# Kernel optimization log

Measured on AMD Instinct MI355X. Metric: run time of the kernel, lower is better.

The kernel has to match this reference:

```python
import jax, jax.numpy as jnp
import numpy as np

B, C, F, COUP, NBL = 8192, 512, 8, 1024, 2
D1 = C - C // 2   # 256, split_len1 (FrEIA AllInOneBlock)
D2 = C // 2       # 256, split_len2
CLAMP = 2.0       # FrEIA affine clamping default
G_INIT = 0.2 * np.log(np.exp(5.0) - 1.0)  # param init s.t. global scale activation == 1.0


def setup_inputs() -> dict:
    key = jax.random.key(0)
    ks = jax.random.split(key, 10)
    z0 = jax.random.normal(ks[0], (B, C), jnp.float32)
    # random orthogonal soft-permutation matrix per flow (permute_soft=True)
    A = jax.random.normal(ks[1], (F, C, C), jnp.float32)
    Wp, _ = jnp.linalg.qr(A)
    g = jnp.float32(G_INIT) + 0.05 * jax.random.normal(ks[2], (F, C), jnp.float32)
    off = 0.01 * jax.random.normal(ks[3], (F, C), jnp.float32)
    s0 = np.float32(1.0 / np.sqrt(D1))
    sh = np.float32(1.0 / np.sqrt(COUP))
    w0 = s0 * jax.random.normal(ks[4], (F, COUP, D1), jnp.float32)
    b0 = s0 * jax.random.normal(ks[5], (F, COUP), jnp.float32)
    wh = sh * jax.random.normal(ks[6], (F, NBL, COUP, COUP), jnp.float32)
    bh = sh * jax.random.normal(ks[7], (F, NBL, COUP), jnp.float32)
    wo = sh * jax.random.normal(ks[8], (F, 2 * D2, COUP), jnp.float32)
    bo = sh * jax.random.normal(ks[9], (F, 2 * D2), jnp.float32)
    return dict(z0=z0, Wp=Wp, g=g, off=off, w0=w0, b0=b0, wh=wh, bh=bh, wo=wo, bo=bo)


def _subnet(x1, w0, b0, wh, bh, wo, bo):
    # Linear(D1, COUP) -> ReLU -> [Linear(COUP, COUP) -> ReLU]*NBL -> Linear(COUP, 2*D2)
    h = jax.nn.relu(x1 @ w0.T + b0)
    for i in range(NBL):
        h = jax.nn.relu(h @ wh[i].T + bh[i])
    return h @ wo.T + bo


def reference(z0, Wp, g, off, w0, b0, wh, bh, wo, bo):
    def block(carry, p):
        x, ld = carry
        Wp_, g_, off_, w0_, b0_, wh_, bh_, wo_, bo_ = p
        # global affine: scale = 0.1 * softplus_{beta=0.5}(g) = 0.2 * softplus(0.5*g)
        scale = 0.2 * jax.nn.softplus(0.5 * g_)
        x = (x * scale + off_) @ Wp_.T            # soft permutation: F.linear(x, W)
        x1, x2 = x[:, :D1], x[:, D1:]
        a = 0.1 * _subnet(x1, w0_, b0_, wh_, bh_, wo_, bo_)
        s = CLAMP * jnp.tanh(a[:, :D2])
        t = a[:, D2:]
        x2 = x2 * jnp.exp(s) + t
        ld = ld + jnp.sum(s, axis=1) + jnp.sum(jnp.log(scale))
        return (jnp.concatenate([x1, x2], axis=1), ld), None

    init = (z0, jnp.zeros((z0.shape[0],), z0.dtype))
    (zk, log_det), _ = jax.lax.scan(block, init, (Wp, g, off, w0, b0, wh, bh, wo, bo))
    return zk, log_det
```

## Files before the change

### kernel.cpp

```cpp
#include <hip/hip_runtime.h>
#include <stdint.h>
#include <stddef.h>

#define B_    8192
#define C_    512
#define F_    8
#define COUP_ 1024
#define NBL_  2
#define D1_   256
#define D2_   256

typedef __attribute__((ext_vector_type(8))) short   short8;
typedef __attribute__((ext_vector_type(4))) float   floatx4;
typedef __attribute__((ext_vector_type(8))) int     int8v;
typedef __attribute__((ext_vector_type(4))) int     int4v;

__device__ __forceinline__ unsigned short f2bf(float f) {
  unsigned int u = __float_as_uint(f);
  unsigned int r = (u + 0x7fffu + ((u >> 16) & 1u)) >> 16;
  return (unsigned short)r;
}

#if __has_builtin(__builtin_amdgcn_cvt_pk_fp8_f32)
__device__ __forceinline__ unsigned char f2fp8(float f) {
  return (unsigned char)(__builtin_amdgcn_cvt_pk_fp8_f32(f, f, 0, false) & 0xFF);
}
__device__ __forceinline__ unsigned int f2fp8x4(float4 v) {
  int r = __builtin_amdgcn_cvt_pk_fp8_f32(v.x, v.y, 0, false);
  r = __builtin_amdgcn_cvt_pk_fp8_f32(v.z, v.w, r, true);
  return (unsigned int)r;
}
#else
__device__ __forceinline__ unsigned char f2fp8(float f) {
  unsigned int fu = __float_as_uint(f);
  unsigned char s = (unsigned char)((fu >> 24) & 0x80u);
  float a = fabsf(f);
  if (!(a >= 0.015625f)) {
    int m = (int)rintf(a * 512.0f);
    return s | (unsigned char)m;
  }
  if (a > 448.0f) return s | 0x7E;
  unsigned int u = __float_as_uint(a);
  int e = (int)((u >> 23) & 0xFF) - 127;
  unsigned int mant = u & 0x7FFFFFu;
  unsigned int r = mant >> 20;
  unsigned int rest = mant & 0xFFFFFu;
  if (rest > 0x80000u || (rest == 0x80000u && (r & 1u))) r++;
  if (r == 8u) { r = 0u; e++; }
  if (e > 8) { e = 8; r = 7u; }
  return s | (unsigned char)(((unsigned)(e + 7) << 3) | r);
}
__device__ __forceinline__ unsigned int f2fp8x4(float4 v) {
  uchar4 o;
  o.x = f2fp8(v.x); o.y = f2fp8(v.y); o.z = f2fp8(v.z); o.w = f2fp8(v.w);
  return *(unsigned int*)&o;
}
#endif

__device__ __forceinline__ void gload_lds16(const void* g, void* l) {
  void* gnc = const_cast<void*>(g);
  __builtin_amdgcn_global_load_lds(
      (__attribute__((address_space(1))) void*)gnc,
      (__attribute__((address_space(3))) void*)l, 16, 0, 0);
}

__device__ __forceinline__ int8v read_frag8(const unsigned char* lbase, int rr, int q) {
  const int j  = rr & 7;
  const int c0 = (2 * q) ^ j;
  const unsigned char* b = lbase + (rr >> 3) * 1024 + j * 128;
  int4v lo = *(const int4v*)(b + c0 * 16);
  int4v hi = *(const int4v*)(b + (c0 ^ 1) * 16);
  return __builtin_shufflevector(lo, hi, 0, 1, 2, 3, 4, 5, 6, 7);
}

__global__ __launch_bounds__(128, 2)
void gemm_wp(const unsigned short* __restrict__ A,
             const unsigned short* __restrict__ W,
             float* __restrict__ outF,
             unsigned char* __restrict__ outB,
             int M, int N, int K)
{
  __shared__ __align__(16) unsigned short lA[128 * 32];
  __shared__ __align__(16) unsigned short lB[64 * 32];
  const int tid  = threadIdx.x;
  const int wave = tid >> 6;
  const int lane = tid & 63;
  const int bm = blockIdx.y * 128;
  const int bn = blockIdx.x * 64;
  const int wm = wave * 64;

  floatx4 acc[4][4];
#pragma unroll
  for (int i = 0; i < 4; ++i)
#pragma unroll
    for (int j = 0; j < 4; ++j)
      acc[i][j] = (floatx4){0.f, 0.f, 0.f, 0.f};

  const int srow  = lane >> 2;
  const int skoff = (lane & 3) * 8;
  const unsigned short* ga = A + (size_t)(bm + wave * 64 + srow) * K + skoff;
  const unsigned short* gb = W + (size_t)(bn + wave * 32 + srow) * K + skoff;
  unsigned short* laB = &lA[(wave * 64) * 32];
  unsigned short* lbB = &lB[(wave * 32) * 32];
  const size_t rowstep = (size_t)16 * K;

  const int q8 = (lane >> 4) * 8;
  const int r  = lane & 15;

  for (int k0 = 0; k0 < K; k0 += 32) {
    if (k0) __syncthreads();
    gload_lds16(ga,               laB);
    gload_lds16(ga + rowstep,     laB + 16 * 32);
    gload_lds16(ga + 2 * rowstep, laB + 32 * 32);
    gload_lds16(ga + 3 * rowstep, laB + 48 * 32);
    gload_lds16(gb,               lbB);
    gload_lds16(gb + rowstep,     lbB + 16 * 32);
    ga += 32; gb += 32;
    __syncthreads();

    short8 af[4], bf[4];
#pragma unroll
    for (int t = 0; t < 4; ++t)
      af[t] = *(const short8*)&lA[(wm + t * 16 + r) * 32 + q8];
#pragma unroll
    for (int t = 0; t < 4; ++t)
      bf[t] = *(const short8*)&lB[(t * 16 + r) * 32 + q8];

#pragma unroll
    for (int i = 0; i < 4; ++i)
#pragma unroll
      for (int j = 0; j < 4; ++j)
        acc[i][j] = __builtin_amdgcn_mfma_f32_16x16x32_bf16(af[i], bf[j], acc[i][j], 0, 0, 0);
  }

  const int q4 = (lane >> 4) * 4;
  const int cc = lane & 15;
#pragma unroll
  for (int i = 0; i < 4; ++i) {
    const int row0 = bm + wm + i * 16 + q4;
#pragma unroll
    for (int j = 0; j < 4; ++j) {
      const int col = bn + j * 16 + cc;
#pragma unroll
      for (int rr = 0; rr < 4; ++rr) {
        const int row = row0 + rr;
        float v = acc[i][j][rr];
        outF[(size_t)row * 512 + col] = v;
        if (col < D1_) outB[(size_t)row * D1_ + col] = f2fp8(v);
      }
    }
  }
}

__global__ __launch_bounds__(256, 2)
void gemm_f8(const unsigned char* __restrict__ A,
             const unsigned char* __restrict__ W,
             const float* __restrict__ bias,
             unsigned char* __restrict__ outB,
             int M, int N, int K)
{
  __shared__ __align__(16) unsigned char lA[128 * 128];
  __shared__ __align__(16) unsigned char lB[128 * 128];
  const int tid  = threadIdx.x;
  const int wave = tid >> 6;
  const int lane = tid & 63;
  const int bm = blockIdx.y * 128;
  const int bn = blockIdx.x * 128;
  const int wm = (wave & 1) * 64;
  const int wn = (wave >> 1) * 64;

  floatx4 acc[4][4];
#pragma unroll
  for (int i = 0; i < 4; ++i)
#pragma unroll
    for (int j = 0; j < 4; ++j)
      acc[i][j] = (floatx4){0.f, 0.f, 0.f, 0.f};

  const int jj = lane >> 3;
  const int chunkoff = ((lane & 7) ^ jj) * 16;
  const unsigned char* gA = A + (size_t)(bm + jj) * K + chunkoff;
  const unsigned char* gB = W + (size_t)(bn + jj) * K + chunkoff;

  const int q = lane >> 4;
  const int r = lane & 15;

  for (int k0 = 0; k0 < K; k0 += 128) {
    if (k0) __syncthreads();
#pragma unroll
    for (int ii = 0; ii < 4; ++ii) {
      const int i = 4 * wave + ii;
      gload_lds16(gA + (size_t)(8 * i) * K + k0, &lA[i * 1024]);
      gload_lds16(gB + (size_t)(8 * i) * K + k0, &lB[i * 1024]);
    }
    __syncthreads();

    int8v af[4], bfv[4];
#pragma unroll
    for (int t = 0; t < 4; ++t) af[t]  = read_frag8(lA, wm + t * 16 + r, q);
#pragma unroll
    for (int t = 0; t < 4; ++t) bfv[t] = read_frag8(lB, wn + t * 16 + r, q);

#pragma unroll
    for (int i = 0; i < 4; ++i)
#pragma unroll
      for (int j = 0; j < 4; ++j)
        acc[i][j] = __builtin_amdgcn_mfma_scale_f32_16x16x128_f8f6f4(
            af[i], bfv[j], acc[i][j], 0, 0, 0, 0x7f7f7f7f, 0, 0x7f7f7f7f);
  }

  const int q4 = (lane >> 4) * 4;
  const int cc = lane & 15;
#pragma unroll
  for (int i = 0; i < 4; ++i) {
    const int row0 = bm + wm + i * 16 + q4;
#pragma unroll
    for (int j = 0; j < 4; ++j) {
      const int col = bn + wn + j * 16 + cc;
      const float bv = bias[col];
#pragma unroll
      for (int rr = 0; rr < 4; ++rr) {
        float v = acc[i][j][rr] + bv;
        v = v > 0.f ? v : 0.f;
        outB[(size_t)(row0 + rr) * N + col] = f2fp8(v);
      }
    }
  }
}

__global__ __launch_bounds__(128, 2)
void gemm_f8_wo(const unsigned char* __restrict__ A,
                const unsigned char* __restrict__ W,
                const float* __restrict__ bias,
                float* __restrict__ outF,
                int M, int N, int K)
{
  __shared__ __align__(16) unsigned char lA[128 * 128];
  __shared__ __align__(16) unsigned char lB[64 * 128];
  const int tid  = threadIdx.x;
  const int wave = tid >> 6;
  const int lane = tid & 63;
  const int bm = blockIdx.y * 128;
  const int bn = blockIdx.x * 64;
  const int wm = wave * 64;

  floatx4 acc[4][4];
#pragma unroll
  for (int i = 0; i < 4; ++i)
#pragma unroll
    for (int j = 0; j < 4; ++j)
      acc[i][j] = (floatx4){0.f, 0.f, 0.f, 0.f};

  const int jj = lane >> 3;
  const int chunkoff = ((lane & 7) ^ jj) * 16;
  const unsigned char* gA = A + (size_t)(bm + jj) * K + chunkoff;
  const unsigned char* gB = W + (size_t)(bn + jj) * K + chunkoff;

  const int q = lane >> 4;
  const int r = lane & 15;

  for (int k0 = 0; k0 < K; k0 += 128) {
    if (k0) __syncthreads();
#pragma unroll
    for (int ii = 0; ii < 8; ++ii) {
      const int i = 8 * wave + ii;
      gload_lds16(gA + (size_t)(8 * i) * K + k0, &lA[i * 1024]);
    }
#pragma unroll
    for (int ii = 0; ii < 4; ++ii) {
      const int i = 4 * wave + ii;
      gload_lds16(gB + (size_t)(8 * i) * K + k0, &lB[i * 1024]);
    }
    __syncthreads();

    int8v af[4], bfv[4];
#pragma unroll
    for (int t = 0; t < 4; ++t) af[t]  = read_frag8(lA, wm + t * 16 + r, q);
#pragma unroll
    for (int t = 0; t < 4; ++t) bfv[t] = read_frag8(lB, t * 16 + r, q);

#pragma unroll
    for (int i = 0; i < 4; ++i)
#pragma unroll
      for (int j = 0; j < 4; ++j)
        acc[i][j] = __builtin_amdgcn_mfma_scale_f32_16x16x128_f8f6f4(
            af[i], bfv[j], acc[i][j], 0, 0, 0, 0x7f7f7f7f, 0, 0x7f7f7f7f);
  }

  const int q4 = (lane >> 4) * 4;
  const int cc = lane & 15;
#pragma unroll
  for (int i = 0; i < 4; ++i) {
    const int row0 = bm + wm + i * 16 + q4;
#pragma unroll
    for (int j = 0; j < 4; ++j) {
      const int col = bn + j * 16 + cc;
      const float bv = bias[col];
#pragma unroll
      for (int rr = 0; rr < 4; ++rr)
        outF[(size_t)(row0 + rr) * 512 + col] = 0.1f * (acc[i][j][rr] + bv);
    }
  }
}

__global__ void scale_kernel(const float* __restrict__ g, float* __restrict__ sc,
                             float* __restrict__ sumlog) {
  const int f = blockIdx.x, t = threadIdx.x;
  __shared__ float red[256];
  float part = 0.f;
  for (int c = t; c < C_; c += 256) {
    float x  = 0.5f * g[f * C_ + c];
    float sp = log1pf(expf(x));
    float s  = 0.2f * sp;
    sc[f * C_ + c] = s;
    part += logf(s);
  }
  red[t] = part;
  __syncthreads();
  for (int o = 128; o > 0; o >>= 1) {
    if (t < o) red[t] += red[t + o];
    __syncthreads();
  }
  if (t == 0) sumlog[f] = red[0];
}

__global__ void cvt4_kernel(const float* __restrict__ s0, unsigned short* __restrict__ d0, int n0,
                            const float* __restrict__ s1, unsigned char* __restrict__ d1, int n1,
                            const float* __restrict__ s2, unsigned char* __restrict__ d2, int n2,
                            const float* __restrict__ s3, unsigned char* __restrict__ d3, int n3) {
  const int total4 = (n0 + n1 + n2 + n3) >> 2;
  for (int i = blockIdx.x * blockDim.x + threadIdx.x; i < total4;
       i += gridDim.x * blockDim.x) {
    int idx = i << 2;
    if (idx < n0) {
      float4 v = *(const float4*)(s0 + idx);
      ushort4 o;
      o.x = f2bf(v.x); o.y = f2bf(v.y); o.z = f2bf(v.z); o.w = f2bf(v.w);
      *(ushort4*)(d0 + idx) = o;
    } else {
      const float* s; unsigned char* d; int off;
      if (idx < n0 + n1)           { s = s1; d = d1; off = idx - n0; }
      else if (idx < n0 + n1 + n2) { s = s2; d = d2; off = idx - n0 - n1; }
      else                         { s = s3; d = d3; off = idx - n0 - n1 - n2; }
      *(unsigned int*)(d + off) = f2fp8x4(*(const float4*)(s + off));
    }
  }
}

__global__ void prewp_kernel(const float* __restrict__ x, const float* __restrict__ sc,
                             const float* __restrict__ off, unsigned short* __restrict__ xb,
                             float* __restrict__ ld) {
  int i = blockIdx.x * blockDim.x + threadIdx.x;
  if (i < B_ / 4) *(float4*)(ld + i * 4) = (float4){0.f, 0.f, 0.f, 0.f};
  if (i >= (B_ * C_) / 4) return;
  int idx = i << 2;
  int c = idx & (C_ - 1);
  float4 v = *(const float4*)(x + idx);
  float4 s = *(const float4*)(sc + c);
  float4 o = *(const float4*)(off + c);
  ushort4 r;
  r.x = f2bf(v.x * s.x + o.x);
  r.y = f2bf(v.y * s.y + o.y);
  r.z = f2bf(v.z * s.z + o.z);
  r.w = f2bf(v.w * s.w + o.w);
  *(ushort4*)(xb + idx) = r;
}

template<int LAST>
__global__ __launch_bounds__(256)
void couple_kernel(const float* __restrict__ a, float* __restrict__ xst,
                   float* __restrict__ ld,
                   const float* __restrict__ scn, const float* __restrict__ offn,
                   unsigned short* __restrict__ xb,
                   const float* __restrict__ sumlog, float* __restrict__ ldout) {
  const int wave = threadIdx.x >> 6, lane = threadIdx.x & 63;
  const int row = blockIdx.x * 4 + wave;
  const float* ar = a + (size_t)row * 512;
  float* xr = xst + (size_t)row * C_;
  float nx2[4];
  float ssum = 0.f;
#pragma unroll
  for (int it = 0; it < 4; ++it) {
    int j = it * 64 + lane;
    float s = 2.0f * tanhf(ar[j]);
    float t = ar[D2_ + j];
    float v = xr[D1_ + j] * expf(s) + t;
    xr[D1_ + j] = v;
    nx2[it] = v;
    ssum += s;
  }
#pragma unroll
  for (int o = 32; o > 0; o >>= 1) ssum += __shfl_down(ssum, o, 64);
  if (!LAST) {
    if (lane == 0) ld[row] += ssum;
    unsigned short* xbr = xb + (size_t)row * C_;
#pragma unroll
    for (int it = 0; it < 4; ++it) {
      int c = it * 64 + lane;
      xbr[c] = f2bf(xr[c] * scn[c] + offn[c]);
    }
#pragma unroll
    for (int it = 0; it < 4; ++it) {
      int c = D1_ + it * 64 + lane;
      xbr[c] = f2bf(nx2[it] * scn[c] + offn[c]);
    }
  } else {
    if (lane == 0) {
      float t = 0.f;
#pragma unroll
      for (int f = 0; f < F_; ++f) t += sumlog[f];
      ldout[row] = ld[row] + ssum + t;
    }
  }
}

extern "C" void kernel_launch(void* const* d_in, const int* in_sizes, int n_in,
                              void* d_out, int out_size, void* d_ws, size_t ws_size,
                              hipStream_t stream) {
  const float* z0  = (const float*)d_in[0];
  const float* Wp  = (const float*)d_in[1];
  const float* g   = (const float*)d_in[2];
  const float* off = (const float*)d_in[3];
  const float* w0  = (const float*)d_in[4];
  const float* b0  = (const float*)d_in[5];
  const float* wh  = (const float*)d_in[6];
  const float* bh  = (const float*)d_in[7];
  const float* wo  = (const float*)d_in[8];
  const float* bo  = (const float*)d_in[9];
  float* out = (float*)d_out;

  char* ws = (char*)d_ws;
  size_t p = 0;
  auto alloc = [&](size_t bytes) -> void* {
    p = (p + 255) & ~(size_t)255;
    void* r = ws + p;
    p += bytes;
    return r;
  };
  float* sc           = (float*)alloc((size_t)F_ * C_ * 4);
  float* sumlog       = (float*)alloc((size_t)F_ * 4);
  float* ld           = (float*)alloc((size_t)B_ * 4);
  float* xst          = (float*)alloc((size_t)B_ * C_ * 4);
  unsigned short* xb  = (unsigned short*)alloc((size_t)B_ * C_ * 2);
  unsigned char* x1f8 = (unsigned char*)alloc((size_t)B_ * D1_);
  unsigned char* h1f8 = (unsigned char*)alloc((size_t)B_ * COUP_);
  unsigned char* h2f8 = (unsigned char*)alloc((size_t)B_ * COUP_);
  float* abuf         = (float*)alloc((size_t)B_ * 512 * 4);
  unsigned short* wpb = (unsigned short*)alloc((size_t)F_ * C_ * C_ * 2);
  unsigned char* w0f8 = (unsigned char*)alloc((size_t)F_ * COUP_ * D1_);
  unsigned char* whf8 = (unsigned char*)alloc((size_t)F_ * NBL_ * COUP_ * COUP_);
  unsigned char* wof8 = (unsigned char*)alloc((size_t)F_ * 2 * D2_ * COUP_);
  (void)ws_size; (void)in_sizes; (void)n_in; (void)out_size;

  scale_kernel<<<F_, 256, 0, stream>>>(g, sc, sumlog);

  cvt4_kernel<<<2048, 256, 0, stream>>>(
      Wp, wpb, F_ * C_ * C_,
      w0, w0f8, F_ * COUP_ * D1_,
      wh, whf8, F_ * NBL_ * COUP_ * COUP_,
      wo, wof8, F_ * 2 * D2_ * COUP_);

  prewp_kernel<<<(B_ * C_ / 4) / 256, 256, 0, stream>>>(z0, sc, off, xb, ld);

  for (int f = 0; f < F_; ++f) {
    const int last = (f == F_ - 1);
    gemm_wp<<<dim3(512 / 64, B_ / 128), 128, 0, stream>>>(
        xb, wpb + (size_t)f * C_ * C_, last ? out : xst, x1f8, B_, 512, 512);

    gemm_f8<<<dim3(COUP_ / 128, B_ / 128), 256, 0, stream>>>(
        x1f8, w0f8 + (size_t)f * COUP_ * D1_, b0 + (size_t)f * COUP_,
        h1f8, B_, COUP_, D1_);

    gemm_f8<<<dim3(COUP_ / 128, B_ / 128), 256, 0, stream>>>(
        h1f8, whf8 + (size_t)(f * NBL_) * COUP_ * COUP_,
        bh + (size_t)(f * NBL_ + 0) * COUP_, h2f8, B_, COUP_, COUP_);

    gemm_f8<<<dim3(COUP_ / 128, B_ / 128), 256, 0, stream>>>(
        h2f8, whf8 + (size_t)(f * NBL_ + 1) * COUP_ * COUP_,
        bh + (size_t)(f * NBL_ + 1) * COUP_, h1f8, B_, COUP_, COUP_);

    gemm_f8_wo<<<dim3(512 / 64, B_ / 128), 128, 0, stream>>>(
        h1f8, wof8 + (size_t)f * 2 * D2_ * COUP_, bo + (size_t)f * 2 * D2_,
        abuf, B_, 512, COUP_);

    if (!last) {
      couple_kernel<0><<<B_ / 4, 256, 0, stream>>>(
          abuf, xst, ld, sc + (size_t)(f + 1) * C_, off + (size_t)(f + 1) * C_,
          xb, nullptr, nullptr);
    } else {
      couple_kernel<1><<<B_ / 4, 256, 0, stream>>>(
          abuf, out, ld, nullptr, nullptr, nullptr, sumlog, out + (size_t)B_ * C_);
    }
  }
}
```

Before: 797.9 us.

## Fuse affine coupling into output GEMM epilogue and prescale x1 in permutation GEMM

Removes the standalone coupling kernel and the fp32 subnet-output buffer. The output GEMM now pairs each s-column with its matching t-column inside one block, so it can apply tanh, exp and the affine update in its epilogue. It also writes the next flow's bf16 input and accumulates per-column-block log-det partials. The permutation GEMM writes the scaled-and-offset bf16 x1 half for the next flow directly, and ping-pong input buffers avoid read/write hazards. This saves a full read/write round trip of intermediate activations per flow, at the cost of heavier epilogues, scattered 2-byte stores, and a final reduction kernel.

```diff
diff --git a/kernel.cpp b/kernel.cpp
--- a/kernel.cpp
+++ b/kernel.cpp
@@ -73,11 +73,14 @@
   return __builtin_shufflevector(lo, hi, 0, 1, 2, 3, 4, 5, 6, 7);
 }
 
+template<int LASTF>
 __global__ __launch_bounds__(128, 2)
 void gemm_wp(const unsigned short* __restrict__ A,
              const unsigned short* __restrict__ W,
              float* __restrict__ outF,
              unsigned char* __restrict__ outB,
+             const float* __restrict__ scn, const float* __restrict__ offn,
+             unsigned short* __restrict__ xbn,
              int M, int N, int K)
 {
   __shared__ __align__(16) unsigned short lA[128 * 32];
@@ -145,8 +148,16 @@
       for (int rr = 0; rr < 4; ++rr) {
         const int row = row0 + rr;
         float v = acc[i][j][rr];
-        outF[(size_t)row * 512 + col] = v;
-        if (col < D1_) outB[(size_t)row * D1_ + col] = f2fp8(v);
+        if (LASTF) {
+          outF[(size_t)row * 512 + col] = v;
+        } else if (col >= D1_) {
+          outF[(size_t)row * 512 + col] = v;
+        }
+        if (col < D1_) {
+          outB[(size_t)row * D1_ + col] = f2fp8(v);
+          if (!LASTF)
+            xbn[(size_t)row * C_ + col] = f2bf(v * scn[col] + offn[col]);
+        }
       }
     }
   }
@@ -227,21 +238,26 @@
   }
 }
 
+template<int LASTF>
 __global__ __launch_bounds__(128, 2)
-void gemm_f8_wo(const unsigned char* __restrict__ A,
-                const unsigned char* __restrict__ W,
-                const float* __restrict__ bias,
-                float* __restrict__ outF,
-                int M, int N, int K)
+void gemm_wo_couple(const unsigned char* __restrict__ A,
+                    const unsigned char* __restrict__ W,
+                    const float* __restrict__ bias,
+                    const float* __restrict__ xst,
+                    float* __restrict__ outF,
+                    const float* __restrict__ scn, const float* __restrict__ offn,
+                    unsigned short* __restrict__ xbn,
+                    float* __restrict__ ldpart,
+                    int M, int K)
 {
   __shared__ __align__(16) unsigned char lA[128 * 128];
   __shared__ __align__(16) unsigned char lB[64 * 128];
   const int tid  = threadIdx.x;
   const int wave = tid >> 6;
   const int lane = tid & 63;
-  const int bm = blockIdx.y * 128;
-  const int bn = blockIdx.x * 64;
-  const int wm = wave * 64;
+  const int bm  = blockIdx.y * 128;
+  const int bnp = blockIdx.x;
+  const int wm  = wave * 64;
 
   floatx4 acc[4][4];
 #pragma unroll
@@ -253,7 +269,8 @@
   const int jj = lane >> 3;
   const int chunkoff = ((lane & 7) ^ jj) * 16;
   const unsigned char* gA = A + (size_t)(bm + jj) * K + chunkoff;
-  const unsigned char* gB = W + (size_t)(bn + jj) * K + chunkoff;
+  const unsigned char* gB =
+      W + (size_t)((wave ? 256 : 0) + 32 * bnp + jj) * K + chunkoff;
 
   const int q = lane >> 4;
   const int r = lane & 15;
@@ -267,8 +284,7 @@
     }
 #pragma unroll
     for (int ii = 0; ii < 4; ++ii) {
-      const int i = 4 * wave + ii;
-      gload_lds16(gB + (size_t)(8 * i) * K + k0, &lB[i * 1024]);
+      gload_lds16(gB + (size_t)(8 * ii) * K + k0, &lB[(4 * wave + ii) * 1024]);
     }
     __syncthreads();
 
@@ -288,18 +304,49 @@
 
   const int q4 = (lane >> 4) * 4;
   const int cc = lane & 15;
+  float ssum[4][4];
+#pragma unroll
+  for (int i = 0; i < 4; ++i)
+#pragma unroll
+    for (int rr = 0; rr < 4; ++rr) ssum[i][rr] = 0.f;
+
 #pragma unroll
   for (int i = 0; i < 4; ++i) {
     const int row0 = bm + wm + i * 16 + q4;
 #pragma unroll
-    for (int j = 0; j < 4; ++j) {
-      const int col = bn + j * 16 + cc;
-      const float bv = bias[col];
-#pragma unroll
-      for (int rr = 0; rr < 4; ++rr)
-        outF[(size_t)(row0 + rr) * 512 + col] = 0.1f * (acc[i][j][rr] + bv);
-    }
-  }
+    for (int jjp = 0; jjp < 2; ++jjp) {
+      const int cp = 32 * bnp + jjp * 16 + cc;
+      const float bs = bias[cp];
+      const float bt = bias[256 + cp];
+#pragma unroll
+      for (int rr = 0; rr < 4; ++rr) {
+        const int row = row0 + rr;
+        float sa = 0.1f * (acc[i][jjp][rr] + bs);
+        float ta = 0.1f * (acc[i][jjp + 2][rr] + bt);
+        float s  = 2.0f * tanhf(sa);
+        float x2n = xst[(size_t)row * 512 + 256 + cp] * expf(s) + ta;
+        if (LASTF) {
+          outF[(size_t)row * 512 + 256 + cp] = x2n;
+        } else {
+          xbn[(size_t)row * C_ + D1_ + cp] = f2bf(x2n * scn[D1_ + cp] + offn[D1_ + cp]);
+        }
+        ssum[i][rr] += s;
+      }
+    }
+  }
+
+#pragma unroll
+  for (int i = 0; i < 4; ++i)
+#pragma unroll
+    for (int rr = 0; rr < 4; ++rr) {
+      float v = ssum[i][rr];
+#pragma unroll
+      for (int m = 1; m < 16; m <<= 1) v += __shfl_xor(v, m, 64);
+      if (cc == 0) {
+        const int row = bm + wm + i * 16 + q4 + rr;
+        ldpart[(size_t)bnp * B_ + row] += v;
+      }
+    }
 }
 
 __global__ void scale_kernel(const float* __restrict__ g, float* __restrict__ sc,
@@ -348,9 +395,9 @@
 
 __global__ void prewp_kernel(const float* __restrict__ x, const float* __restrict__ sc,
                              const float* __restrict__ off, unsigned short* __restrict__ xb,
-                             float* __restrict__ ld) {
+                             float* __restrict__ ldpart) {
   int i = blockIdx.x * blockDim.x + threadIdx.x;
-  if (i < B_ / 4) *(float4*)(ld + i * 4) = (float4){0.f, 0.f, 0.f, 0.f};
+  if (i < (8 * B_) / 4) *(float4*)(ldpart + i * 4) = (float4){0.f, 0.f, 0.f, 0.f};
   if (i >= (B_ * C_) / 4) return;
   int idx = i << 2;
   int c = idx & (C_ - 1);
@@ -365,52 +412,18 @@
   *(ushort4*)(xb + idx) = r;
 }
 
-template<int LAST>
-__global__ __launch_bounds__(256)
-void couple_kernel(const float* __restrict__ a, float* __restrict__ xst,
-                   float* __restrict__ ld,
-                   const float* __restrict__ scn, const float* __restrict__ offn,
-                   unsigned short* __restrict__ xb,
-                   const float* __restrict__ sumlog, float* __restrict__ ldout) {
-  const int wave = threadIdx.x >> 6, lane = threadIdx.x & 63;
-  const int row = blockIdx.x * 4 + wave;
-  const float* ar = a + (size_t)row * 512;
-  float* xr = xst + (size_t)row * C_;
-  float nx2[4];
-  float ssum = 0.f;
-#pragma unroll
-  for (int it = 0; it < 4; ++it) {
-    int j = it * 64 + lane;
-    float s = 2.0f * tanhf(ar[j]);
-    float t = ar[D2_ + j];
-    float v = xr[D1_ + j] * expf(s) + t;
-    xr[D1_ + j] = v;
-    nx2[it] = v;
-    ssum += s;
-  }
-#pragma unroll
-  for (int o = 32; o > 0; o >>= 1) ssum += __shfl_down(ssum, o, 64);
-  if (!LAST) {
-    if (lane == 0) ld[row] += ssum;
-    unsigned short* xbr = xb + (size_t)row * C_;
-#pragma unroll
-    for (int it = 0; it < 4; ++it) {
-      int c = it * 64 + lane;
-      xbr[c] = f2bf(xr[c] * scn[c] + offn[c]);
-    }
-#pragma unroll
-    for (int it = 0; it < 4; ++it) {
-      int c = D1_ + it * 64 + lane;
-      xbr[c] = f2bf(nx2[it] * scn[c] + offn[c]);
-    }
-  } else {
-    if (lane == 0) {
-      float t = 0.f;
-#pragma unroll
-      for (int f = 0; f < F_; ++f) t += sumlog[f];
-      ldout[row] = ld[row] + ssum + t;
-    }
-  }
+__global__ void final_ld_kernel(const float* __restrict__ ldpart,
+                                const float* __restrict__ sumlog,
+                                float* __restrict__ ldout) {
+  int row = blockIdx.x * blockDim.x + threadIdx.x;
+  if (row >= B_) return;
+  float t = 0.f;
+#pragma unroll
+  for (int f = 0; f < F_; ++f) t += sumlog[f];
+  float v = 0.f;
+#pragma unroll
+  for (int nb = 0; nb < 8; ++nb) v += ldpart[(size_t)nb * B_ + row];
+  ldout[row] = v + t;
 }
 
 extern "C" void kernel_launch(void* const* d_in, const int* in_sizes, int n_in,
@@ -438,13 +451,13 @@
   };
   float* sc           = (float*)alloc((size_t)F_ * C_ * 4);
   float* sumlog       = (float*)alloc((size_t)F_ * 4);
-  float* ld           = (float*)alloc((size_t)B_ * 4);
+  float* ldpart       = (float*)alloc((size_t)8 * B_ * 4);
   float* xst          = (float*)alloc((size_t)B_ * C_ * 4);
-  unsigned short* xb  = (unsigned short*)alloc((size_t)B_ * C_ * 2);
+  unsigned short* xbA = (unsigned short*)alloc((size_t)B_ * C_ * 2);
+  unsigned short* xbB = (unsigned short*)alloc((size_t)B_ * C_ * 2);
   unsigned char* x1f8 = (unsigned char*)alloc((size_t)B_ * D1_);
   unsigned char* h1f8 = (unsigned char*)alloc((size_t)B_ * COUP_);
   unsigned char* h2f8 = (unsigned char*)alloc((size_t)B_ * COUP_);
-  float* abuf         = (float*)alloc((size_t)B_ * 512 * 4);
   unsigned short* wpb = (unsigned short*)alloc((size_t)F_ * C_ * C_ * 2);
   unsigned char* w0f8 = (unsigned char*)alloc((size_t)F_ * COUP_ * D1_);
   unsigned char* whf8 = (unsigned char*)alloc((size_t)F_ * NBL_ * COUP_ * COUP_);
@@ -459,36 +472,46 @@
       wh, whf8, F_ * NBL_ * COUP_ * COUP_,
       wo, wof8, F_ * 2 * D2_ * COUP_);
 
-  prewp_kernel<<<(B_ * C_ / 4) / 256, 256, 0, stream>>>(z0, sc, off, xb, ld);
+  prewp_kernel<<<(B_ * C_ / 4) / 256, 256, 0, stream>>>(z0, sc, off, xbA, ldpart);
 
   for (int f = 0; f < F_; ++f) {
     const int last = (f == F_ - 1);
-    gemm_wp<<<dim3(512 / 64, B_ / 128), 128, 0, stream>>>(
-        xb, wpb + (size_t)f * C_ * C_, last ? out : xst, x1f8, B_, 512, 512);
-
-    gemm_f8<<<dim3(COUP_ / 128, B_ / 128), 256, 0, stream>>>(
+    unsigned short* xbc = (f & 1) ? xbB : xbA;
+    unsigned short* xbn = (f & 1) ? xbA : xbB;
+    const float* scn  = sc  + (size_t)(f + 1) * C_;
+    const float* offn = off + (size_t)(f + 1) * C_;
+
+    if (!last) {
+      gemm_wp<0><<<dim3(8, 64), 128, 0, stream>>>(
+          xbc, wpb + (size_t)f * C_ * C_, xst, x1f8, scn, offn, xbn, B_, 512, 512);
+    } else {
+      gemm_wp<1><<<dim3(8, 64), 128, 0, stream>>>(
+          xbc, wpb + (size_t)f * C_ * C_, out, x1f8, nullptr, nullptr, nullptr,
+          B_, 512, 512);
+    }
+
+    gemm_f8<<<dim3(8, 64), 256, 0, stream>>>(
         x1f8, w0f8 + (size_t)f * COUP_ * D1_, b0 + (size_t)f * COUP_,
         h1f8, B_, COUP_, D1_);
 
-    gemm_f8<<<dim3(COUP_ / 128, B_ / 128), 256, 0, stream>>>(
+    gemm_f8<<<dim3(8, 64), 256, 0, stream>>>(
         h1f8, whf8 + (size_t)(f * NBL_) * COUP_ * COUP_,
         bh + (size_t)(f * NBL_ + 0) * COUP_, h2f8, B_, COUP_, COUP_);
 
-    gemm_f8<<<dim3(COUP_ / 128, B_ / 128), 256, 0, stream>>>(
+    gemm_f8<<<dim3(8, 64), 256, 0, stream>>>(
         h2f8, whf8 + (size_t)(f * NBL_ + 1) * COUP_ * COUP_,
         bh + (size_t)(f * NBL_ + 1) * COUP_, h1f8, B_, COUP_, COUP_);
 
-    gemm_f8_wo<<<dim3(512 / 64, B_ / 128), 128, 0, stream>>>(
-        h1f8, wof8 + (size_t)f * 2 * D2_ * COUP_, bo + (size_t)f * 2 * D2_,
-        abuf, B_, 512, COUP_);
-
     if (!last) {
-      couple_kernel<0><<<B_ / 4, 256, 0, stream>>>(
-          abuf, xst, ld, sc + (size_t)(f + 1) * C_, off + (size_t)(f + 1) * C_,
-          xb, nullptr, nullptr);
+      gemm_wo_couple<0><<<dim3(8, 64), 128, 0, stream>>>(
+          h1f8, wof8 + (size_t)f * 2 * D2_ * COUP_, bo + (size_t)f * 2 * D2_,
+          last ? out : xst, nullptr, scn, offn, xbn, ldpart, B_, COUP_);
     } else {
-      couple_kernel<1><<<B_ / 4, 256, 0, stream>>>(
-          abuf, out, ld, nullptr, nullptr, nullptr, sumlog, out + (size_t)B_ * C_);
-    }
-  }
-}
+      gemm_wo_couple<1><<<dim3(8, 64), 128, 0, stream>>>(
+          h1f8, wof8 + (size_t)f * 2 * D2_ * COUP_, bo + (size_t)f * 2 * D2_,
+          out, out, nullptr, nullptr, nullptr, ldpart, B_, COUP_);
+    }
+  }
+
+  final_ld_kernel<<<B_ / 256, 256, 0, stream>>>(ldpart, sumlog, out + (size_t)B_ * C_);
+}
```

Result: slower. 863.8 us (+8.3%).
